# Performance work log

Hardware: AMD Instinct MI355X
Metric: run time of the kernel (lower is better)

The kernel has to match this reference:

```python
import jax, jax.numpy as jnp
import numpy as np

NUM_ITERATIONS = 3


def _squash(t, axis=-1):
    sq = jnp.sum(t * t, axis=axis, keepdims=True)
    return (sq / (1.0 + sq)) * t / jnp.sqrt(sq)


def setup_inputs() -> dict:
    key = jax.random.key(0)
    k1, k2 = jax.random.split(key)
    B, R, CIN = 256, 1152, 8
    NCAPS, COUT = 10, 16
    x = jax.random.normal(k1, (B, R, CIN), dtype=jnp.float32)
    route_weights = jax.random.normal(k2, (NCAPS, R, CIN, COUT), dtype=jnp.float32)
    return {"x": x, "route_weights": route_weights}


def reference(x, route_weights):
    # priors: [caps, B, route, 1, out] == x[None,:,:,None,:] @ W[:,None,:,:,:]
    priors = jnp.einsum('bri,crio->cbro', x, route_weights)[:, :, :, None, :]
    logits = jnp.zeros_like(priors)  # [caps, B, route, 1, out]
    outputs = None
    for i in range(NUM_ITERATIONS):
        probs = jax.nn.softmax(logits, axis=2)  # softmax over route nodes
        outputs = _squash(jnp.sum(probs * priors, axis=2, keepdims=True))
        if i != NUM_ITERATIONS - 1:
            logits = logits + jnp.sum(priors * outputs, axis=-1, keepdims=True)
    return outputs  # [caps, B, 1, 1, out]
```

## Files before the change

kernel.cpp:

```cpp
#include <hip/hip_runtime.h>
#include <cstddef>

#define NCAPS  10
#define BATCH  256
#define NROUTE 1152
#define CIN    8
#define COUT   16
#define T      1024
#define NB     4
#define NWAVE  (T / 64)
#define NBLK   (NCAPS * (BATCH / NB))
#define PLANE  (NROUTE * 8)
#define XPLANE (NROUTE * CIN)

__device__ __forceinline__ unsigned swzu(unsigned unit) { return unit ^ ((unit >> 3) & 3u); }

__device__ __forceinline__ unsigned pack_bf16(float a, float b) {
    unsigned ua = __float_as_uint(a); ua += 0x7fffu + ((ua >> 16) & 1u);
    unsigned ub = __float_as_uint(b); ub += 0x7fffu + ((ub >> 16) & 1u);
    return (ua >> 16) | (ub & 0xffff0000u);
}
__device__ __forceinline__ float blo(unsigned u) { return __uint_as_float(u << 16); }
__device__ __forceinline__ float bhi(unsigned u) { return __uint_as_float(u & 0xffff0000u); }

__device__ __forceinline__ float wave_sum(float v) {
    v += __shfl_xor(v, 1);  v += __shfl_xor(v, 2);  v += __shfl_xor(v, 4);
    v += __shfl_xor(v, 8);  v += __shfl_xor(v, 16); v += __shfl_xor(v, 32);
    return v;
}

__device__ __forceinline__ float wave_sum16(float* s, int lane) {
#pragma unroll
    for (int j = 0; j < 8; ++j) {
        float snd = (lane & 1) ? s[j] : s[j + 8];
        float r = __shfl_xor(snd, 1);
        s[j] = ((lane & 1) ? s[j + 8] : s[j]) + r;
    }
#pragma unroll
    for (int j = 0; j < 4; ++j) {
        float snd = (lane & 2) ? s[j] : s[j + 4];
        float r = __shfl_xor(snd, 2);
        s[j] = ((lane & 2) ? s[j + 4] : s[j]) + r;
    }
#pragma unroll
    for (int j = 0; j < 2; ++j) {
        float snd = (lane & 4) ? s[j] : s[j + 2];
        float r = __shfl_xor(snd, 4);
        s[j] = ((lane & 4) ? s[j + 2] : s[j]) + r;
    }
    {
        float snd = (lane & 8) ? s[0] : s[1];
        float r = __shfl_xor(snd, 8);
        s[0] = ((lane & 8) ? s[1] : s[0]) + r;
    }
    s[0] += __shfl_xor(s[0], 16);
    s[0] += __shfl_xor(s[0], 32);
    return s[0];
}

union U4 { uint4 v; unsigned u[4]; };
union U2 { uint2 v; unsigned u[2]; };

__device__ __forceinline__ void phaseA_unit(int u, const float* __restrict__ Wc,
                                            const float* __restrict__ xb,
                                            unsigned* prLDS) {
    const int r = u >> 3;
    const int j = u & 7;
    float xs[NB][CIN];
#pragma unroll
    for (int b = 0; b < NB; ++b) {
        const float4* xq = (const float4*)(xb + (size_t)b * XPLANE + r * CIN);
        float4 xa = xq[0], xv = xq[1];
        xs[b][0] = xa.x; xs[b][1] = xa.y; xs[b][2] = xa.z; xs[b][3] = xa.w;
        xs[b][4] = xv.x; xs[b][5] = xv.y; xs[b][6] = xv.z; xs[b][7] = xv.w;
    }
    float2 acc[NB];
#pragma unroll
    for (int b = 0; b < NB; ++b) { acc[b].x = 0.f; acc[b].y = 0.f; }
    const float* wq = Wc + (size_t)r * (CIN * COUT) + j * 2;
#pragma unroll
    for (int i = 0; i < CIN; ++i) {
        float2 w = *(const float2*)(wq + i * COUT);
#pragma unroll
        for (int b = 0; b < NB; ++b) {
            acc[b].x = fmaf(xs[b][i], w.x, acc[b].x);
            acc[b].y = fmaf(xs[b][i], w.y, acc[b].y);
        }
    }
    const unsigned base = swzu(2u * (unsigned)r + (unsigned)(j >> 2)) * 4u + (unsigned)(j & 3);
#pragma unroll
    for (int b = 0; b < NB; ++b)
        prLDS[b * PLANE + base] = pack_bf16(acc[b].x, acc[b].y);
}

__global__ __launch_bounds__(T) void caps_routing(const float* __restrict__ x,
                                                  const float* __restrict__ W,
                                                  float* __restrict__ out) {
    __shared__ unsigned prLDS[NB * PLANE];
    __shared__ float sred[NWAVE][20];
    __shared__ __align__(16) float VLDS[NB][COUT];

    const int tid  = threadIdx.x;
    const int lane = tid & 63;
    const int wv   = tid >> 6;

    int g    = blockIdx.x;
    int widx = (g & 7) * (NBLK / 8) + (g >> 3);
    int c    = widx >> 6;
    int b0   = (widx & 63) * NB;

    const float* Wc = W + (size_t)c * (NROUTE * CIN * COUT);
    const float* xb = x + (size_t)b0 * XPLANE;

#pragma unroll 1
    for (int pass = 0; pass < (NROUTE * 8) / T; ++pass) {
        phaseA_unit(pass * T + tid, Wc, xb, prLDS);
    }
    __syncthreads();

    const int bb   = wv >> 2;
    const int t256 = ((wv & 3) << 6) | lane;
    const int h    = t256 & 1;
    const int r2   = 1024 + (t256 >> 1);
    const unsigned pbase = (unsigned)bb * PLANE;
    const int comp = ((lane & 1) << 3) | ((lane & 2) << 1) | ((lane & 4) >> 1) | ((lane & 8) >> 3);

#pragma unroll 1
    for (int it = 0; it < 3; ++it) {
        float s16[COUT];
        float se = 0.f;
#pragma unroll
        for (int o = 0; o < COUT; ++o) s16[o] = 0.f;

#pragma unroll
        for (int q = 0; q < 4; ++q) {
            const int r = (q << 8) + t256;
            const unsigned d0 = pbase + swzu(2u * (unsigned)r) * 4u;
            const unsigned d1 = pbase + swzu(2u * (unsigned)r + 1u) * 4u;
            U4 qa, qb;
            qa.v = *(const uint4*)&prLDS[d0];
            qb.v = *(const uint4*)&prLDS[d1];
            float p[COUT];
#pragma unroll
            for (int u = 0; u < 4; ++u) {
                p[2 * u]     = blo(qa.u[u]);  p[2 * u + 1] = bhi(qa.u[u]);
                p[8 + 2 * u] = blo(qb.u[u]);  p[9 + 2 * u] = bhi(qb.u[u]);
            }
            float e;
            if (it > 0) {
                float d = 0.f;
#pragma unroll
                for (int u = 0; u < 4; ++u) {
                    float4 v4 = *(const float4*)&VLDS[bb][4 * u];
                    d = fmaf(p[4 * u + 0], v4.x, d);
                    d = fmaf(p[4 * u + 1], v4.y, d);
                    d = fmaf(p[4 * u + 2], v4.z, d);
                    d = fmaf(p[4 * u + 3], v4.w, d);
                }
                e = __expf(d);
            } else {
                e = 1.f;
            }
            se += e;
#pragma unroll
            for (int o = 0; o < COUT; ++o) s16[o] = fmaf(e, p[o], s16[o]);
        }

        {
            const unsigned dw = pbase + swzu(2u * (unsigned)r2 + (unsigned)h) * 4u;
            U4 q;
            q.v = *(const uint4*)&prLDS[dw];
            float pl[8];
#pragma unroll
            for (int u = 0; u < 4; ++u) { pl[2 * u] = blo(q.u[u]); pl[2 * u + 1] = bhi(q.u[u]); }
            float e2;
            if (it > 0) {
                float d2 = 0.f;
#pragma unroll
                for (int j = 0; j < 8; ++j) d2 = fmaf(pl[j], VLDS[bb][h * 8 + j], d2);
                d2 += __shfl_xor(d2, 1);
                e2 = __expf(d2);
            } else {
                e2 = 1.f;
            }
            se += 0.5f * e2;
#pragma unroll
            for (int j = 0; j < 8; ++j) {
                const float add = e2 * pl[j];
                s16[j]     += (h == 0) ? add : 0.f;
                s16[8 + j] += (h == 1) ? add : 0.f;
            }
        }

        const float sv  = wave_sum16(s16, lane);
        const float sev = wave_sum(se);
        if (lane < 16) sred[wv][comp] = sv;
        if (lane == 0) sred[wv][16]   = sev;
        __syncthreads();

        if (tid < NB * COUT) {
            const int b = tid >> 4, o = tid & 15;
            float S = 0.f, SE = 0.f;
#pragma unroll
            for (int k = 0; k < 4; ++k) {
                S  += sred[b * 4 + k][o];
                SE += sred[b * 4 + k][16];
            }
            const float tt = S / SE;
            float pq = tt * tt;
            pq += __shfl_xor(pq, 1); pq += __shfl_xor(pq, 2);
            pq += __shfl_xor(pq, 4); pq += __shfl_xor(pq, 8);
            const float scale = pq / ((1.f + pq) * sqrtf(pq));
            const float val = tt * scale;
            if (it == 2) {
                out[((size_t)c * BATCH + b0 + b) * COUT + o] = val;
            } else {
                VLDS[b][o] = (it == 0) ? val : (VLDS[b][o] + val);
            }
        }
        __syncthreads();
    }
}

extern "C" void kernel_launch(void* const* d_in, const int* in_sizes, int n_in,
                              void* d_out, int out_size, void* d_ws, size_t ws_size,
                              hipStream_t stream) {
    const float* x = (const float*)d_in[0];
    const float* w = (const float*)d_in[1];
    float* out = (float*)d_out;
    hipLaunchKernelGGL(caps_routing, dim3(NBLK), dim3(T), 0, stream, x, w, out);
}
```

Baseline: 81.96 us.

## Shrink block to 2 batches x 768 threads and keep priors in registers across iterations

Each block now handles 2 batch items with 768 threads (384 per batch), so every thread owns exactly 3 route nodes. The half-route tail path with its shuffle goes away. The bf16 priors are loaded from LDS once into registers before the routing loop and reused in all three iterations. The dot product is split into two accumulators, and log2e is folded into the stored V so exp2f can replace __expf. The grid doubles to 1280 blocks with half the LDS each, which changes occupancy, and the cost is more register pressure from holding 6 uint4 values per thread.

```diff
diff --git a/kernel.cpp b/kernel.cpp
--- a/kernel.cpp
+++ b/kernel.cpp
@@ -6,12 +6,13 @@
 #define NROUTE 1152
 #define CIN    8
 #define COUT   16
-#define T      1024
-#define NB     4
+#define T      768
+#define NB     2
 #define NWAVE  (T / 64)
 #define NBLK   (NCAPS * (BATCH / NB))
 #define PLANE  (NROUTE * 8)
 #define XPLANE (NROUTE * CIN)
+#define LOG2E  1.4426950408889634f
 
 __device__ __forceinline__ unsigned swzu(unsigned unit) { return unit ^ ((unit >> 3) & 3u); }
 
@@ -59,7 +60,6 @@
 }
 
 union U4 { uint4 v; unsigned u[4]; };
-union U2 { uint2 v; unsigned u[2]; };
 
 __device__ __forceinline__ void phaseA_unit(int u, const float* __restrict__ Wc,
                                             const float* __restrict__ xb,
@@ -93,6 +93,32 @@
         prLDS[b * PLANE + base] = pack_bf16(acc[b].x, acc[b].y);
 }
 
+__device__ __forceinline__ void routeBody(const U4& qa, const U4& qb, int it,
+                                          const float* Vt, float* s16, float& se) {
+    float e;
+    if (it > 0) {
+        float d0 = 0.f, d1 = 0.f;
+#pragma unroll
+        for (int q = 0; q < 4; ++q) {
+            d0 = fmaf(blo(qa.u[q]), Vt[2 * q],     d0);
+            d1 = fmaf(bhi(qa.u[q]), Vt[2 * q + 1], d1);
+            d0 = fmaf(blo(qb.u[q]), Vt[8 + 2 * q], d0);
+            d1 = fmaf(bhi(qb.u[q]), Vt[9 + 2 * q], d1);
+        }
+        e = exp2f(d0 + d1);
+    } else {
+        e = 1.f;
+    }
+    se += e;
+#pragma unroll
+    for (int q = 0; q < 4; ++q) {
+        s16[2 * q]     = fmaf(e, blo(qa.u[q]), s16[2 * q]);
+        s16[2 * q + 1] = fmaf(e, bhi(qa.u[q]), s16[2 * q + 1]);
+        s16[8 + 2 * q] = fmaf(e, blo(qb.u[q]), s16[8 + 2 * q]);
+        s16[9 + 2 * q] = fmaf(e, bhi(qb.u[q]), s16[9 + 2 * q]);
+    }
+}
+
 __global__ __launch_bounds__(T) void caps_routing(const float* __restrict__ x,
                                                   const float* __restrict__ W,
                                                   float* __restrict__ out) {
@@ -106,8 +132,8 @@
 
     int g    = blockIdx.x;
     int widx = (g & 7) * (NBLK / 8) + (g >> 3);
-    int c    = widx >> 6;
-    int b0   = (widx & 63) * NB;
+    int c    = widx >> 7;
+    int b0   = (widx & 127) * NB;
 
     const float* Wc = W + (size_t)c * (NROUTE * CIN * COUT);
     const float* xb = x + (size_t)b0 * XPLANE;
@@ -118,12 +144,23 @@
     }
     __syncthreads();
 
-    const int bb   = wv >> 2;
-    const int t256 = ((wv & 3) << 6) | lane;
-    const int h    = t256 & 1;
-    const int r2   = 1024 + (t256 >> 1);
+    const int bb   = (tid >= 384) ? 1 : 0;
+    const int t384 = tid - 384 * bb;
     const unsigned pbase = (unsigned)bb * PLANE;
     const int comp = ((lane & 1) << 3) | ((lane & 2) << 1) | ((lane & 4) >> 1) | ((lane & 8) >> 3);
+
+    U4 qa0, qb0, qa1, qb1, qa2, qb2;
+    {
+        const unsigned r0 = (unsigned)t384;
+        const unsigned r1 = (unsigned)t384 + 384u;
+        const unsigned r2 = (unsigned)t384 + 768u;
+        qa0.v = *(const uint4*)&prLDS[pbase + swzu(2u * r0) * 4u];
+        qb0.v = *(const uint4*)&prLDS[pbase + swzu(2u * r0 + 1u) * 4u];
+        qa1.v = *(const uint4*)&prLDS[pbase + swzu(2u * r1) * 4u];
+        qb1.v = *(const uint4*)&prLDS[pbase + swzu(2u * r1 + 1u) * 4u];
+        qa2.v = *(const uint4*)&prLDS[pbase + swzu(2u * r2) * 4u];
+        qb2.v = *(const uint4*)&prLDS[pbase + swzu(2u * r2 + 1u) * 4u];
+    }
 
 #pragma unroll 1
     for (int it = 0; it < 3; ++it) {
@@ -132,65 +169,10 @@
 #pragma unroll
         for (int o = 0; o < COUT; ++o) s16[o] = 0.f;
 
-#pragma unroll
-        for (int q = 0; q < 4; ++q) {
-            const int r = (q << 8) + t256;
-            const unsigned d0 = pbase + swzu(2u * (unsigned)r) * 4u;
-            const unsigned d1 = pbase + swzu(2u * (unsigned)r + 1u) * 4u;
-            U4 qa, qb;
-            qa.v = *(const uint4*)&prLDS[d0];
-            qb.v = *(const uint4*)&prLDS[d1];
-            float p[COUT];
-#pragma unroll
-            for (int u = 0; u < 4; ++u) {
-                p[2 * u]     = blo(qa.u[u]);  p[2 * u + 1] = bhi(qa.u[u]);
-                p[8 + 2 * u] = blo(qb.u[u]);  p[9 + 2 * u] = bhi(qb.u[u]);
-            }
-            float e;
-            if (it > 0) {
-                float d = 0.f;
-#pragma unroll
-                for (int u = 0; u < 4; ++u) {
-                    float4 v4 = *(const float4*)&VLDS[bb][4 * u];
-                    d = fmaf(p[4 * u + 0], v4.x, d);
-                    d = fmaf(p[4 * u + 1], v4.y, d);
-                    d = fmaf(p[4 * u + 2], v4.z, d);
-                    d = fmaf(p[4 * u + 3], v4.w, d);
-                }
-                e = __expf(d);
-            } else {
-                e = 1.f;
-            }
-            se += e;
-#pragma unroll
-            for (int o = 0; o < COUT; ++o) s16[o] = fmaf(e, p[o], s16[o]);
-        }
-
-        {
-            const unsigned dw = pbase + swzu(2u * (unsigned)r2 + (unsigned)h) * 4u;
-            U4 q;
-            q.v = *(const uint4*)&prLDS[dw];
-            float pl[8];
-#pragma unroll
-            for (int u = 0; u < 4; ++u) { pl[2 * u] = blo(q.u[u]); pl[2 * u + 1] = bhi(q.u[u]); }
-            float e2;
-            if (it > 0) {
-                float d2 = 0.f;
-#pragma unroll
-                for (int j = 0; j < 8; ++j) d2 = fmaf(pl[j], VLDS[bb][h * 8 + j], d2);
-                d2 += __shfl_xor(d2, 1);
-                e2 = __expf(d2);
-            } else {
-                e2 = 1.f;
-            }
-            se += 0.5f * e2;
-#pragma unroll
-            for (int j = 0; j < 8; ++j) {
-                const float add = e2 * pl[j];
-                s16[j]     += (h == 0) ? add : 0.f;
-                s16[8 + j] += (h == 1) ? add : 0.f;
-            }
-        }
+        const float* Vt = &VLDS[bb][0];
+        routeBody(qa0, qb0, it, Vt, s16, se);
+        routeBody(qa1, qb1, it, Vt, s16, se);
+        routeBody(qa2, qb2, it, Vt, s16, se);
 
         const float sv  = wave_sum16(s16, lane);
         const float sev = wave_sum(se);
@@ -202,9 +184,9 @@
             const int b = tid >> 4, o = tid & 15;
             float S = 0.f, SE = 0.f;
 #pragma unroll
-            for (int k = 0; k < 4; ++k) {
-                S  += sred[b * 4 + k][o];
-                SE += sred[b * 4 + k][16];
+            for (int w = 0; w < 6; ++w) {
+                S  += sred[b * 6 + w][o];
+                SE += sred[b * 6 + w][16];
             }
             const float tt = S / SE;
             float pq = tt * tt;
@@ -215,7 +197,8 @@
             if (it == 2) {
                 out[((size_t)c * BATCH + b0 + b) * COUT + o] = val;
             } else {
-                VLDS[b][o] = (it == 0) ? val : (VLDS[b][o] + val);
+                const float vt = val * LOG2E;
+                VLDS[b][o] = (it == 0) ? vt : (VLDS[b][o] + vt);
             }
         }
         __syncthreads();
```

Result: slower. 98.50 us (+20.2%).
